# Performance work log

Hardware: AMD Instinct MI355X
Metric: run time of the kernel (lower is better)

## Reference

```python
import jax, jax.numpy as jnp
import numpy as np

N_NODES = 100000
N_EDGES = 1600000
IN_FEATS = 128
N_HIDDEN = 64
N_HEADS = 4
N_CLASSES = 16


def setup_inputs() -> dict:
    key = jax.random.key(0)
    ks = jax.random.split(key, 16)
    h = jax.random.normal(ks[0], (N_NODES, IN_FEATS), dtype=jnp.float32)
    src = jax.random.randint(ks[1], (N_EDGES,), 0, N_NODES, dtype=jnp.int32)
    dst = jax.random.randint(ks[2], (N_EDGES,), 0, N_NODES, dtype=jnp.int32)
    def xavier(k, shape, fan_in, fan_out):
        gain = jnp.sqrt(2.0)  # calculate_gain('relu')
        std = gain * jnp.sqrt(2.0 / (fan_in + fan_out))
        return (std * jax.random.normal(k, shape)).astype(jnp.float32)
    # layer 1: per-head W [H, in, out], A [H, 2*out]
    W1 = xavier(ks[3], (N_HEADS, IN_FEATS, N_HIDDEN), IN_FEATS, N_HIDDEN)
    b1 = jnp.zeros((N_HEADS, N_HIDDEN), jnp.float32)
    a1 = xavier(ks[4], (N_HEADS, 2 * N_HIDDEN), 2 * N_HIDDEN, 1)
    ab1 = jnp.zeros((N_HEADS,), jnp.float32)
    # layer 2: input is concat of heads = N_HEADS*N_HIDDEN, output n_classes, heads averaged
    d2 = N_HEADS * N_HIDDEN
    W2 = xavier(ks[5], (N_HEADS, d2, N_CLASSES), d2, N_CLASSES)
    b2 = jnp.zeros((N_HEADS, N_CLASSES), jnp.float32)
    a2 = xavier(ks[6], (N_HEADS, 2 * N_CLASSES), 2 * N_CLASSES, 1)
    ab2 = jnp.zeros((N_HEADS,), jnp.float32)
    fc_w = xavier(ks[7], (N_CLASSES, N_CLASSES), N_CLASSES, N_CLASSES)
    fc_b = jnp.zeros((N_CLASSES,), jnp.float32)
    return dict(h=h, src=src, dst=dst, W1=W1, b1=b1, a1=a1, ab1=ab1,
                W2=W2, b2=b2, a2=a2, ab2=ab2, fc_w=fc_w, fc_b=fc_b)


def gat_layer(h, src, dst, W, b, a, ab, n_nodes):
    # h: [N, F]; W: [H, F, O]; a: [H, 2O]
    O = W.shape[-1]
    Wh = jnp.einsum('nf,hfo->nho', h, W) + b          # [N, H, O]
    Wh_src = Wh[src]                                   # [E, H, O] (messages Wh_j)
    Wh_dst = Wh[dst]                                   # [E, H, O] (Wh_i)
    # e_ij = LeakyReLU(A([Wh_i, Wh_j]), 0.2)
    e = (jnp.einsum('eho,ho->eh', Wh_dst, a[:, :O])
         + jnp.einsum('eho,ho->eh', Wh_src, a[:, O:]) + ab)  # [E, H]
    e = jax.nn.leaky_relu(e, 0.2)
    # segment softmax over incoming edges of each dst node
    m = jax.ops.segment_max(e, dst, num_segments=n_nodes)     # [N, H] (-inf for empty)
    ex = jnp.exp(e - m[dst])
    denom = jax.ops.segment_sum(ex, dst, num_segments=n_nodes)
    alpha = ex / denom[dst]                                    # [E, H]
    # weighted neighbor aggregation (zero for zero-in-degree nodes, as DGL)
    out = jax.ops.segment_sum(alpha[:, :, None] * Wh_src, dst, num_segments=n_nodes)
    return out  # [N, H, O]


def reference(h, src, dst, W1, b1, a1, ab1, W2, b2, a2, ab2, fc_w, fc_b):
    n = h.shape[0]
    # layer 1 (heads concatenated) + ELU; dropout = identity (eval mode)
    h1 = gat_layer(h, src, dst, W1, b1, a1, ab1, n)            # [N, H, n_hidden]
    h1 = jax.nn.elu(h1.reshape(n, -1))                         # [N, H*n_hidden]
    # layer 2 (heads averaged) + softmax over features
    h2 = gat_layer(h1, src, dst, W2, b2, a2, ab2, n).mean(axis=1)  # [N, n_classes]
    h2 = jax.nn.softmax(h2, axis=1)
    # readout: mean over nodes, then fc
    hg = h2.mean(axis=0)                                        # [n_classes]
    return hg @ fc_w.T + fc_b
```

## Files before the change

### kernel.cpp

```cpp
#include <hip/hip_runtime.h>
#include <math.h>

#define N_NODES  100000
#define N_EDGES  1600000
#define IN_F     128
#define HID      64
#define HEADS    4
#define NCLS     16
#define D1       (HEADS*HID)
#define D2       (HEADS*NCLS)

#define RB1 128
#define AGG_BLOCKS 2048
#define AGG_WAVES  (AGG_BLOCKS * 4)
#define GEMM1_BLOCKS ((N_NODES + 63) / 64)

#define NBKT   ((N_NODES + 255) / 256)
#define BCAP   5120
#define BK_BLOCKS 256
#define BK_CHUNK  ((N_EDGES + BK_BLOCKS - 1) / BK_BLOCKS)

typedef __attribute__((ext_vector_type(8))) short bf16x8_t;
typedef __attribute__((ext_vector_type(4))) float f32x4_t;
typedef __attribute__((ext_vector_type(2))) float f32x2_t;

__device__ __forceinline__ unsigned bf16rne(float x) {
  unsigned u = __float_as_uint(x);
  return (u + 0x7fffu + ((u >> 16) & 1u)) >> 16;
}
__device__ __forceinline__ unsigned packbf2(float lo, float hi) {
  return bf16rne(lo) | (bf16rne(hi) << 16);
}
__device__ __forceinline__ f32x2_t pkfma(f32x2_t a, f32x2_t b, f32x2_t c) {
  return __builtin_elementwise_fma(a, b, c);
}

__global__ __launch_bounds__(256)
void k_prep(const float* __restrict__ W1, const float* __restrict__ W2,
            unsigned* __restrict__ W1t32, unsigned* __restrict__ W2t32,
            int* __restrict__ cursor) {
  int t = threadIdx.x;
  if (blockIdx.x == 0) {
    int c = t;
    const float* wp = W1 + ((c >> 6) << 13) + (c & 63);
    unsigned* op = W1t32 + c * 64;
    for (int fp = 0; fp < 64; ++fp) {
      float lo = wp[(2 * fp) << 6];
      float hi = wp[(2 * fp + 1) << 6];
      op[fp] = packbf2(lo, hi);
    }
  } else if (blockIdx.x == 1) {
    int c = t & 63, fq = t >> 6;
    const float* wp = W2 + ((c >> 4) << 12) + (c & 15);
    unsigned* op = W2t32 + c * 128 + fq * 32;
    for (int fp = 0; fp < 32; ++fp) {
      int f0 = fq * 64 + 2 * fp;
      op[fp] = packbf2(wp[f0 << 4], wp[(f0 + 1) << 4]);
    }
  } else {
    for (int i = t; i <= NBKT; i += 256) cursor[i] = 0;
  }
}

__global__ __launch_bounds__(256)
void k_bucket(const int* __restrict__ src, const int* __restrict__ dst,
              int* __restrict__ cursor, unsigned* __restrict__ bucketed) {
  __shared__ int dstL[BK_CHUNK];
  __shared__ int srcL[BK_CHUNK];
  __shared__ int hist[NBKT];
  __shared__ int base[NBKT];
  __shared__ int cur[NBKT];
  int t = threadIdx.x;
  int e0 = blockIdx.x * BK_CHUNK;
  int e1 = e0 + BK_CHUNK; if (e1 > N_EDGES) e1 = N_EDGES;
  int n = e1 - e0;
  for (int i = t; i < NBKT; i += 256) { hist[i] = 0; cur[i] = 0; }
  __syncthreads();
  for (int i = t; i < n; i += 256) {
    int d = dst[e0 + i];
    int s = src[e0 + i];
    dstL[i] = d;
    srcL[i] = s;
    atomicAdd(&hist[d >> 8], 1);
  }
  __syncthreads();
  for (int i = t; i < NBKT; i += 256) {
    int hv = hist[i];
    base[i] = hv ? atomicAdd(&cursor[i], hv) : 0;
  }
  __syncthreads();
  for (int i = t; i < n; i += 256) {
    int d = dstL[i];
    int b = d >> 8;
    int r = atomicAdd(&cur[b], 1);
    unsigned q = (unsigned)(base[b] + r);
    if (q < BCAP)
      bucketed[(size_t)b * BCAP + q] = ((unsigned)(d & 255) << 20) | (unsigned)srcL[i];
  }
}

__global__ __launch_bounds__(512)
void k_bscan(const int* __restrict__ cursor, int* __restrict__ bbase,
             int* __restrict__ offs) {
  __shared__ int part[512];
  int t = threadIdx.x;
  part[t] = (t < NBKT) ? cursor[t] : 0;
  __syncthreads();
  for (int o = 1; o < 512; o <<= 1) {
    int v = (t >= o) ? part[t - o] : 0;
    __syncthreads();
    part[t] += v;
    __syncthreads();
  }
  if (t < NBKT) bbase[t] = (t == 0) ? 0 : part[t - 1];
  if (t == 0) offs[N_NODES] = N_EDGES;
}

__global__ __launch_bounds__(256)
void k_b2csr(const unsigned* __restrict__ bucketed, const int* __restrict__ cursor,
             const int* __restrict__ bbase,
             int* __restrict__ offs, int* __restrict__ csrsrc) {
  __shared__ unsigned ed[BCAP];
  __shared__ int cnt[256];
  __shared__ int pfx[256];
  __shared__ int exc[256];
  __shared__ int cur[256];
  int b = blockIdx.x;
  int t = threadIdx.x;
  int n = cursor[b]; if (n > BCAP) n = BCAP;
  int gb = bbase[b];
  const unsigned* bp = bucketed + (size_t)b * BCAP;
  cnt[t] = 0;
  __syncthreads();
  for (int i = t; i < n; i += 256) {
    unsigned v = bp[i];
    ed[i] = v;
    atomicAdd(&cnt[v >> 20], 1);
  }
  __syncthreads();
  int x = cnt[t];
  pfx[t] = x;
  __syncthreads();
  for (int o = 1; o < 256; o <<= 1) {
    int v = (t >= o) ? pfx[t - o] : 0;
    __syncthreads();
    pfx[t] += v;
    __syncthreads();
  }
  int excl = pfx[t] - x;
  int node = b * 256 + t;
  if (node < N_NODES) offs[node] = gb + excl;
  exc[t] = excl;
  cur[t] = 0;
  __syncthreads();
  for (int i = t; i < n; i += 256) {
    unsigned v = ed[i];
    int d = v >> 20;
    int r = atomicAdd(&cur[d], 1);
    csrsrc[gb + exc[d] + r] = (int)(v & 0xFFFFFu);
  }
}

__global__ __launch_bounds__(256)
void k_gemm1(const float* __restrict__ h, const unsigned short* __restrict__ W1t,
             const float* __restrict__ bias, const float* __restrict__ a1,
             unsigned char* __restrict__ Wh8,
             float* __restrict__ sD, float* __restrict__ sS) {
  __shared__ float aLds[512];
  int t = threadIdx.x;
  aLds[t] = a1[t];
  aLds[t + 256] = a1[t + 256];
  __syncthreads();

  int wv = t >> 6;
  int lane = t & 63;
  int m = lane & 15;
  int q8 = (lane >> 4) * 8;
  int node = blockIdx.x * 64 + wv * 16 + m;
  int nclamp = node < N_NODES ? node : N_NODES - 1;

  f32x4_t acc[16] = {};
  const float* hp0 = h + (size_t)nclamp * IN_F + q8;
  #pragma unroll
  for (int ks = 0; ks < 4; ++ks) {
    int kk = ks * 32;
    float4 f0 = *(const float4*)(hp0 + kk);
    float4 f1 = *(const float4*)(hp0 + kk + 4);
    bf16x8_t bf;
    bf[0] = (short)bf16rne(f0.x); bf[1] = (short)bf16rne(f0.y);
    bf[2] = (short)bf16rne(f0.z); bf[3] = (short)bf16rne(f0.w);
    bf[4] = (short)bf16rne(f1.x); bf[5] = (short)bf16rne(f1.y);
    bf[6] = (short)bf16rne(f1.z); bf[7] = (short)bf16rne(f1.w);
    #pragma unroll
    for (int ct = 0; ct < 16; ++ct) {
      bf16x8_t af = *(const bf16x8_t*)(W1t + (ct * 16 + m) * IN_F + kk + q8);
      acc[ct] = __builtin_amdgcn_mfma_f32_16x16x32_bf16(af, bf, acc[ct], 0, 0, 0);
    }
  }
  if (node < N_NODES) {
    unsigned char* op = Wh8 + (size_t)node * D1;
    int quad4 = (lane >> 4) * 4;
    float pd[4] = {}, ps[4] = {};
    #pragma unroll
    for (int ct = 0; ct < 16; ++ct) {
      int c0 = ct * 16 + quad4;
      float4 bb = *(const float4*)(bias + c0);
      float v0 = acc[ct][0] + bb.x, v1 = acc[ct][1] + bb.y;
      float v2 = acc[ct][2] + bb.z, v3 = acc[ct][3] + bb.w;
      int hh = ct >> 2;
      const float* aD = &aLds[hh * 128 + (c0 & 63)];
      pd[hh] += v0 * aD[0] + v1 * aD[1] + v2 * aD[2] + v3 * aD[3];
      ps[hh] += v0 * aD[64] + v1 * aD[65] + v2 * aD[66] + v3 * aD[67];
      int pk = __builtin_amdgcn_cvt_pk_fp8_f32(v0, v1, 0, false);
      pk = __builtin_amdgcn_cvt_pk_fp8_f32(v2, v3, pk, true);
      *(unsigned*)(op + c0) = (unsigned)pk;
    }
    #pragma unroll
    for (int hh = 0; hh < 4; ++hh) {
      pd[hh] += __shfl_xor(pd[hh], 16); pd[hh] += __shfl_xor(pd[hh], 32);
      ps[hh] += __shfl_xor(ps[hh], 16); ps[hh] += __shfl_xor(ps[hh], 32);
    }
    if (lane < 16) {
      ((float4*)sD)[node] = make_float4(pd[0], pd[1], pd[2], pd[3]);
      ((float4*)sS)[node] = make_float4(ps[0], ps[1], ps[2], ps[3]);
    }
  }
}

__global__ __launch_bounds__(256)
void k_gemm2(const unsigned short* __restrict__ h1b, const unsigned short* __restrict__ W2t,
             const float* __restrict__ bias, const float* __restrict__ a2,
             unsigned short* __restrict__ Whb2,
             float* __restrict__ sD, float* __restrict__ sS) {
  __shared__ float aLds[128];
  int t = threadIdx.x;
  if (t < 128) aLds[t] = a2[t];
  __syncthreads();

  int wv = t >> 6;
  int lane = t & 63;
  int m = lane & 15;
  int q8 = (lane >> 4) * 8;
  int node = blockIdx.x * 64 + wv * 16 + m;
  int nclamp = node < N_NODES ? node : N_NODES - 1;

  f32x4_t acc[4] = {};
  const unsigned short* hp0 = h1b + (size_t)nclamp * D1 + q8;
  #pragma unroll
  for (int ks = 0; ks < 8; ++ks) {
    int kk = ks * 32;
    bf16x8_t bf = *(const bf16x8_t*)(hp0 + kk);
    #pragma unroll
    for (int ct = 0; ct < 4; ++ct) {
      bf16x8_t af = *(const bf16x8_t*)(W2t + (ct * 16 + m) * D1 + kk + q8);
      acc[ct] = __builtin_amdgcn_mfma_f32_16x16x32_bf16(af, bf, acc[ct], 0, 0, 0);
    }
  }
  if (node < N_NODES) {
    unsigned short* op = Whb2 + (size_t)node * D2;
    int quad4 = (lane >> 4) * 4;
    float pd[4] = {}, ps[4] = {};
    #pragma unroll
    for (int ct = 0; ct < 4; ++ct) {
      int c0 = ct * 16 + quad4;
      float4 bb = *(const float4*)(bias + c0);
      float v0 = acc[ct][0] + bb.x, v1 = acc[ct][1] + bb.y;
      float v2 = acc[ct][2] + bb.z, v3 = acc[ct][3] + bb.w;
      const float* aD = &aLds[ct * 32 + (c0 & 15)];
      pd[ct] += v0 * aD[0] + v1 * aD[1] + v2 * aD[2] + v3 * aD[3];
      ps[ct] += v0 * aD[16] + v1 * aD[17] + v2 * aD[18] + v3 * aD[19];
      uint2 o;
      o.x = packbf2(v0, v1);
      o.y = packbf2(v2, v3);
      *(uint2*)(op + c0) = o;
    }
    #pragma unroll
    for (int hh = 0; hh < 4; ++hh) {
      pd[hh] += __shfl_xor(pd[hh], 16); pd[hh] += __shfl_xor(pd[hh], 32);
      ps[hh] += __shfl_xor(ps[hh], 16); ps[hh] += __shfl_xor(ps[hh], 32);
    }
    if (lane < 16) {
      ((float4*)sD)[node] = make_float4(pd[0], pd[1], pd[2], pd[3]);
      ((float4*)sS)[node] = make_float4(ps[0], ps[1], ps[2], ps[3]);
    }
  }
}

__device__ __forceinline__ float lrelu(float x) { return x > 0.f ? x : 0.2f * x; }
__device__ __forceinline__ float elu(float x)   { return x > 0.f ? x : expm1f(x); }

__global__ __launch_bounds__(256)
void k_agg1(const int* __restrict__ offs, const int* __restrict__ csrsrc,
            const float* __restrict__ sD, const float* __restrict__ sS,
            const float* __restrict__ ab,
            const unsigned char* __restrict__ Wh8, unsigned short* __restrict__ h1out) {
  __shared__ float exbuf[4][64 * 4];
  __shared__ int   offbuf[4][64];
  int wv = threadIdx.x >> 6;
  int lane = threadIdx.x & 63;
  int g = lane >> 5;
  int l = lane & 31;
  int hh = l >> 3;
  unsigned lb = (unsigned)(l << 3);
  float ab0 = ab[0], ab1 = ab[1], ab2 = ab[2], ab3 = ab[3];
  const float* eb = exbuf[wv];
  const int* ob = offbuf[wv];

  for (int wid = blockIdx.x * 4 + wv; wid < N_NODES; wid += AGG_WAVES) {
    f32x2_t acc[4] = {};
    float z0 = 0.f, z1 = 0.f, z2 = 0.f, z3 = 0.f;
    int beg = offs[wid], end = offs[wid + 1];
    bool nonempty = end > beg;
    if (nonempty) {
      float4 dv = ((const float4*)sD)[wid];
      float db0 = dv.x + ab0, db1 = dv.y + ab1;
      float db2 = dv.z + ab2, db3 = dv.w + ab3;
      for (int cbeg = beg; cbeg < end; cbeg += 64) {
        int j = cbeg + lane;
        int cnt = end - cbeg; if (cnt > 64) cnt = 64;
        int sid = 0;
        float e0 = 0.f, e1 = 0.f, e2 = 0.f, e3 = 0.f;
        if (j < end) {
          sid = csrsrc[j];
          float4 sv = ((const float4*)sS)[sid];
          e0 = __expf(lrelu(db0 + sv.x));
          e1 = __expf(lrelu(db1 + sv.y));
          e2 = __expf(lrelu(db2 + sv.z));
          e3 = __expf(lrelu(db3 + sv.w));
          z0 += e0; z1 += e1; z2 += e2; z3 += e3;
        }
        offbuf[wv][lane] = sid << 8;
        *(float4*)&exbuf[wv][lane * 4] = make_float4(e0, e1, e2, e3);
        int npairs = (cnt + 1) >> 1;
        int nh = (npairs + 1) >> 1;
        for (int u = 0; u < nh; ++u) {
          int iA = 2 * u + g;
          int iB = iA + 2 * nh;
          float wA = eb[iA * 4 + hh];
          float wB = eb[iB * 4 + hh];
          unsigned vA = (unsigned)ob[iA] + lb;
          unsigned vB = (unsigned)ob[iB] + lb;
          uint2 pA = *(const uint2*)(Wh8 + vA);
          uint2 pB = *(const uint2*)(Wh8 + vB);
          f32x2_t wa2 = {wA, wA};
          acc[0] = pkfma(wa2, __builtin_amdgcn_cvt_pk_f32_fp8(pA.x, false), acc[0]);
          acc[1] = pkfma(wa2, __builtin_amdgcn_cvt_pk_f32_fp8(pA.x, true ), acc[1]);
          acc[2] = pkfma(wa2, __builtin_amdgcn_cvt_pk_f32_fp8(pA.y, false), acc[2]);
          acc[3] = pkfma(wa2, __builtin_amdgcn_cvt_pk_f32_fp8(pA.y, true ), acc[3]);
          f32x2_t wb2 = {wB, wB};
          acc[0] = pkfma(wb2, __builtin_amdgcn_cvt_pk_f32_fp8(pB.x, false), acc[0]);
          acc[1] = pkfma(wb2, __builtin_amdgcn_cvt_pk_f32_fp8(pB.x, true ), acc[1]);
          acc[2] = pkfma(wb2, __builtin_amdgcn_cvt_pk_f32_fp8(pB.y, false), acc[2]);
          acc[3] = pkfma(wb2, __builtin_amdgcn_cvt_pk_f32_fp8(pB.y, true ), acc[3]);
        }
      }
      #pragma unroll
      for (int o = 32; o; o >>= 1) {
        z0 += __shfl_xor(z0, o);
        z1 += __shfl_xor(z1, o);
        z2 += __shfl_xor(z2, o);
        z3 += __shfl_xor(z3, o);
      }
    }
    #pragma unroll
    for (int i = 0; i < 4; ++i) {
      acc[i][0] += __shfl_xor(acc[i][0], 32);
      acc[i][1] += __shfl_xor(acc[i][1], 32);
    }
    float z = (hh == 0) ? z0 : (hh == 1) ? z1 : (hh == 2) ? z2 : z3;
    if (!nonempty) z = 1.f;
    float inv = 1.f / z;
    if (g == 0) {
      uint4 o;
      o.x = packbf2(elu(acc[0][0] * inv), elu(acc[0][1] * inv));
      o.y = packbf2(elu(acc[1][0] * inv), elu(acc[1][1] * inv));
      o.z = packbf2(elu(acc[2][0] * inv), elu(acc[2][1] * inv));
      o.w = packbf2(elu(acc[3][0] * inv), elu(acc[3][1] * inv));
      *(uint4*)(h1out + (size_t)wid * D1 + l * 8) = o;
    }
  }
}

__global__ __launch_bounds__(256)
void k_agg2(const int* __restrict__ offs, const int* __restrict__ csrsrc,
            const float* __restrict__ sD, const float* __restrict__ sS,
            const float* __restrict__ ab,
            const unsigned short* __restrict__ Whb2, float* __restrict__ partials) {
  __shared__ float exbuf[4][64 * 4];
  __shared__ int   offbuf[4][64];
  __shared__ float red[4][16];
  int wv = threadIdx.x >> 6;
  int lane = threadIdx.x & 63;
  int g = lane >> 4;
  int l = lane & 15;
  int hh = l >> 2;
  unsigned lb = (unsigned)(l << 3);
  float ab0 = ab[0], ab1 = ab[1], ab2 = ab[2], ab3 = ab[3];
  const float* eb = exbuf[wv];
  const int* ob = offbuf[wv];
  float smacc[4] = {};

  for (int wid = blockIdx.x * 4 + wv; wid < N_NODES; wid += AGG_WAVES) {
    f32x2_t acc[2] = {};
    float z0 = 0.f, z1 = 0.f, z2 = 0.f, z3 = 0.f;
    int beg = offs[wid], end = offs[wid + 1];
    bool nonempty = end > beg;
    if (nonempty) {
      float4 dv = ((const float4*)sD)[wid];
      float db0 = dv.x + ab0, db1 = dv.y + ab1;
      float db2 = dv.z + ab2, db3 = dv.w + ab3;
      for (int cbeg = beg; cbeg < end; cbeg += 64) {
        int j = cbeg + lane;
        int cnt = end - cbeg; if (cnt > 64) cnt = 64;
        int sid = 0;
        float e0 = 0.f, e1 = 0.f, e2 = 0.f, e3 = 0.f;
        if (j < end) {
          sid = csrsrc[j];
          float4 sv = ((const float4*)sS)[sid];
          e0 = __expf(lrelu(db0 + sv.x));
          e1 = __expf(lrelu(db1 + sv.y));
          e2 = __expf(lrelu(db2 + sv.z));
          e3 = __expf(lrelu(db3 + sv.w));
          z0 += e0; z1 += e1; z2 += e2; z3 += e3;
        }
        offbuf[wv][lane] = sid << 7;
        *(float4*)&exbuf[wv][lane * 4] = make_float4(e0, e1, e2, e3);
        int ni = (cnt + 3) >> 2;
        int nh2 = (ni + 1) >> 1;
        for (int it = 0; it < nh2; ++it) {
          int qA = 4 * it + g;
          int qB = qA + 4 * nh2;
          float wA = eb[qA * 4 + hh];
          float wB = eb[qB * 4 + hh];
          unsigned vA = (unsigned)ob[qA] + lb;
          unsigned vB = (unsigned)ob[qB] + lb;
          uint2 pA = *(const uint2*)((const unsigned char*)Whb2 + vA);
          uint2 pB = *(const uint2*)((const unsigned char*)Whb2 + vB);
          f32x2_t wa2 = {wA, wA};
          f32x2_t dA0, dA1;
          dA0[0] = __uint_as_float(pA.x << 16); dA0[1] = __uint_as_float(pA.x & 0xffff0000u);
          dA1[0] = __uint_as_float(pA.y << 16); dA1[1] = __uint_as_float(pA.y & 0xffff0000u);
          acc[0] = pkfma(wa2, dA0, acc[0]);
          acc[1] = pkfma(wa2, dA1, acc[1]);
          f32x2_t wb2 = {wB, wB};
          f32x2_t dB0, dB1;
          dB0[0] = __uint_as_float(pB.x << 16); dB0[1] = __uint_as_float(pB.x & 0xffff0000u);
          dB1[0] = __uint_as_float(pB.y << 16); dB1[1] = __uint_as_float(pB.y & 0xffff0000u);
          acc[0] = pkfma(wb2, dB0, acc[0]);
          acc[1] = pkfma(wb2, dB1, acc[1]);
        }
      }
      #pragma unroll
      for (int s = 32; s; s >>= 1) {
        z0 += __shfl_xor(z0, s);
        z1 += __shfl_xor(z1, s);
        z2 += __shfl_xor(z2, s);
        z3 += __shfl_xor(z3, s);
      }
    }
    #pragma unroll
    for (int i = 0; i < 2; ++i) {
      acc[i][0] += __shfl_xor(acc[i][0], 16);
      acc[i][1] += __shfl_xor(acc[i][1], 16);
      acc[i][0] += __shfl_xor(acc[i][0], 32);
      acc[i][1] += __shfl_xor(acc[i][1], 32);
    }
    float z = (hh == 0) ? z0 : (hh == 1) ? z1 : (hh == 2) ? z2 : z3;
    if (!nonempty) z = 1.f;
    float inv = 1.f / z;
    float val[4];
    val[0] = acc[0][0] * inv;
    val[1] = acc[0][1] * inv;
    val[2] = acc[1][0] * inv;
    val[3] = acc[1][1] * inv;
    #pragma unroll
    for (int i = 0; i < 4; ++i) {
      val[i] += __shfl_xor(val[i], 4);
      val[i] += __shfl_xor(val[i], 8);
      val[i] *= 0.25f;
    }
    float mx = fmaxf(fmaxf(val[0], val[1]), fmaxf(val[2], val[3]));
    mx = fmaxf(mx, __shfl_xor(mx, 1));
    mx = fmaxf(mx, __shfl_xor(mx, 2));
    float e[4];
    float ssum = 0.f;
    #pragma unroll
    for (int i = 0; i < 4; ++i) { e[i] = __expf(val[i] - mx); ssum += e[i]; }
    ssum += __shfl_xor(ssum, 1);
    ssum += __shfl_xor(ssum, 2);
    float rinv = 1.f / ssum;
    #pragma unroll
    for (int i = 0; i < 4; ++i) smacc[i] += e[i] * rinv;
  }

  if (g == 0 && l < 4) {
    #pragma unroll
    for (int i = 0; i < 4; ++i) red[wv][l * 4 + i] = smacc[i];
  }
  __syncthreads();
  if (threadIdx.x < 16) {
    partials[(size_t)blockIdx.x * 16 + threadIdx.x] =
        red[0][threadIdx.x] + red[1][threadIdx.x] +
        red[2][threadIdx.x] + red[3][threadIdx.x];
  }
}

__global__ __launch_bounds__(256)
void k_reduce1(const float* __restrict__ partials, int nrows,
               float* __restrict__ out) {
  __shared__ float red[16][17];
  int t = threadIdx.x;
  int c = t & 15, rl = t >> 4;
  int per = (nrows + RB1 - 1) / RB1;
  int rbeg = blockIdx.x * per;
  int rend = rbeg + per; if (rend > nrows) rend = nrows;
  float s = 0.f;
  for (int r = rbeg + rl; r < rend; r += 16) s += partials[(size_t)r * 16 + c];
  red[rl][c] = s;
  __syncthreads();
  for (int st = 8; st; st >>= 1) {
    if (rl < st) red[rl][c] += red[rl + st][c];
    __syncthreads();
  }
  if (t < 16) out[(size_t)blockIdx.x * 16 + t] = red[0][t];
}

__global__ __launch_bounds__(256)
void k_final(const float* __restrict__ partials,
             const float* __restrict__ fcw, const float* __restrict__ fcb,
             float* __restrict__ out) {
  __shared__ float red[16][17];
  __shared__ float hg[16];
  int t = threadIdx.x;
  int c = t & 15, rl = t >> 4;
  float s = 0.f;
  for (int r = rl; r < RB1; r += 16) s += partials[(size_t)r * 16 + c];
  red[rl][c] = s;
  __syncthreads();
  for (int st = 8; st; st >>= 1) {
    if (rl < st) red[rl][c] += red[rl + st][c];
    __syncthreads();
  }
  if (t < 16) hg[t] = red[0][t] * (1.0f / N_NODES);
  __syncthreads();
  if (t < 16) {
    float acc = fcb[t];
    #pragma unroll
    for (int k = 0; k < 16; ++k) acc += hg[k] * fcw[t * 16 + k];
    out[t] = acc;
  }
}

extern "C" void kernel_launch(void* const* d_in, const int* in_sizes, int n_in,
                              void* d_out, int out_size, void* d_ws, size_t ws_size,
                              hipStream_t stream) {
  const float* h   = (const float*)d_in[0];
  const int*   src = (const int*)  d_in[1];
  const int*   dst = (const int*)  d_in[2];
  const float* W1  = (const float*)d_in[3];
  const float* b1  = (const float*)d_in[4];
  const float* a1  = (const float*)d_in[5];
  const float* ab1 = (const float*)d_in[6];
  const float* W2  = (const float*)d_in[7];
  const float* b2  = (const float*)d_in[8];
  const float* a2  = (const float*)d_in[9];
  const float* ab2 = (const float*)d_in[10];
  const float* fcw = (const float*)d_in[11];
  const float* fcb = (const float*)d_in[12];
  float* out = (float*)d_out;

  char* ws = (char*)d_ws;
  size_t off = 0;
  auto alloc = [&](size_t bytes) -> char* {
    char* p = ws + off;
    off += (bytes + 255) & ~(size_t)255;
    return p;
  };
  unsigned char*  Wh8  = (unsigned char*)alloc((size_t)N_NODES * D1);
  unsigned short* h1b  = (unsigned short*)alloc((size_t)N_NODES * D1 * 2);
  unsigned short* Whb2 = (unsigned short*)alloc((size_t)N_NODES * D2 * 2);
  unsigned short* W1t  = (unsigned short*)alloc((size_t)D1 * IN_F * 2);
  unsigned short* W2t  = (unsigned short*)alloc((size_t)D2 * D1 * 2);
  float* sD1 = (float*)alloc((size_t)N_NODES * 4 * 4);
  float* sS1 = (float*)alloc((size_t)N_NODES * 4 * 4);
  float* sD2 = (float*)alloc((size_t)N_NODES * 4 * 4);
  float* sS2 = (float*)alloc((size_t)N_NODES * 4 * 4);
  int* cursor   = (int*)alloc((size_t)(NBKT + 1) * 4);
  unsigned* bucketed = (unsigned*)alloc((size_t)NBKT * BCAP * 4);
  int* bbase  = (int*)alloc((size_t)NBKT * 4);
  int* offs   = (int*)alloc((size_t)(N_NODES + 1) * 4);
  int* csrsrc = (int*)alloc((size_t)N_EDGES * 4);
  float* partials  = (float*)alloc((size_t)AGG_BLOCKS * 16 * 4);
  float* partials2 = (float*)alloc((size_t)RB1 * 16 * 4);

  k_prep<<<3, 256, 0, stream>>>(W1, W2, (unsigned*)W1t, (unsigned*)W2t, cursor);

  k_bucket<<<BK_BLOCKS, 256, 0, stream>>>(src, dst, cursor, bucketed);

  k_gemm1<<<GEMM1_BLOCKS, 256, 0, stream>>>(h, W1t, b1, a1, Wh8, sD1, sS1);

  k_bscan<<<1, 512, 0, stream>>>(cursor, bbase, offs);
  k_b2csr<<<NBKT, 256, 0, stream>>>(bucketed, cursor, bbase, offs, csrsrc);

  k_agg1<<<AGG_BLOCKS, 256, 0, stream>>>(offs, csrsrc, sD1, sS1, ab1, Wh8, h1b);

  k_gemm2<<<GEMM1_BLOCKS, 256, 0, stream>>>(h1b, W2t, b2, a2, Whb2, sD2, sS2);
  k_agg2<<<AGG_BLOCKS, 256, 0, stream>>>(offs, csrsrc, sD2, sS2, ab2, Whb2, partials);

  k_reduce1<<<RB1, 256, 0, stream>>>(partials, AGG_BLOCKS, partials2);
  k_final<<<1, 256, 0, stream>>>(partials2, fcw, fcb, out);
}
```

Measured before the change: 409.4 us.

## Eliminate scan and reduce kernels by folding work into neighbouring launches

Removes the single-block bucket-scan kernel: each b2csr block now computes its own bucket base by summing the preceding cursor counts with a block reduction, and the offs sentinel is written in k_prep. The two-stage final reduction is merged into one single-block kernel that reads all aggregation partials directly. k_bucket moves to 1024-thread blocks and rereads src/dst from global memory in place of staging them in shared memory. Together these cut two kernel launches and their serialization gaps, at the cost of redundant prefix sums per block, a longer serial final reduction, and a second global read of the edge arrays.

```diff
diff --git a/kernel.cpp b/kernel.cpp
--- a/kernel.cpp
+++ b/kernel.cpp
@@ -10,7 +10,6 @@
 #define D1       (HEADS*HID)
 #define D2       (HEADS*NCLS)
 
-#define RB1 128
 #define AGG_BLOCKS 2048
 #define AGG_WAVES  (AGG_BLOCKS * 4)
 #define GEMM1_BLOCKS ((N_NODES + 63) / 64)
@@ -38,7 +37,7 @@
 __global__ __launch_bounds__(256)
 void k_prep(const float* __restrict__ W1, const float* __restrict__ W2,
             unsigned* __restrict__ W1t32, unsigned* __restrict__ W2t32,
-            int* __restrict__ cursor) {
+            int* __restrict__ cursor, int* __restrict__ offs) {
   int t = threadIdx.x;
   if (blockIdx.x == 0) {
     int c = t;
@@ -59,14 +58,13 @@
     }
   } else {
     for (int i = t; i <= NBKT; i += 256) cursor[i] = 0;
-  }
-}
-
-__global__ __launch_bounds__(256)
+    if (t == 0) offs[N_NODES] = N_EDGES;
+  }
+}
+
+__global__ __launch_bounds__(1024)
 void k_bucket(const int* __restrict__ src, const int* __restrict__ dst,
               int* __restrict__ cursor, unsigned* __restrict__ bucketed) {
-  __shared__ int dstL[BK_CHUNK];
-  __shared__ int srcL[BK_CHUNK];
   __shared__ int hist[NBKT];
   __shared__ int base[NBKT];
   __shared__ int cur[NBKT];
@@ -74,64 +72,50 @@
   int e0 = blockIdx.x * BK_CHUNK;
   int e1 = e0 + BK_CHUNK; if (e1 > N_EDGES) e1 = N_EDGES;
   int n = e1 - e0;
-  for (int i = t; i < NBKT; i += 256) { hist[i] = 0; cur[i] = 0; }
-  __syncthreads();
-  for (int i = t; i < n; i += 256) {
+  for (int i = t; i < NBKT; i += 1024) { hist[i] = 0; cur[i] = 0; }
+  __syncthreads();
+  for (int i = t; i < n; i += 1024)
+    atomicAdd(&hist[dst[e0 + i] >> 8], 1);
+  __syncthreads();
+  for (int i = t; i < NBKT; i += 1024) {
+    int hv = hist[i];
+    base[i] = hv ? atomicAdd(&cursor[i], hv) : 0;
+  }
+  __syncthreads();
+  for (int i = t; i < n; i += 1024) {
     int d = dst[e0 + i];
     int s = src[e0 + i];
-    dstL[i] = d;
-    srcL[i] = s;
-    atomicAdd(&hist[d >> 8], 1);
-  }
-  __syncthreads();
-  for (int i = t; i < NBKT; i += 256) {
-    int hv = hist[i];
-    base[i] = hv ? atomicAdd(&cursor[i], hv) : 0;
-  }
-  __syncthreads();
-  for (int i = t; i < n; i += 256) {
-    int d = dstL[i];
     int b = d >> 8;
     int r = atomicAdd(&cur[b], 1);
     unsigned q = (unsigned)(base[b] + r);
     if (q < BCAP)
-      bucketed[(size_t)b * BCAP + q] = ((unsigned)(d & 255) << 20) | (unsigned)srcL[i];
-  }
-}
-
-__global__ __launch_bounds__(512)
-void k_bscan(const int* __restrict__ cursor, int* __restrict__ bbase,
-             int* __restrict__ offs) {
-  __shared__ int part[512];
-  int t = threadIdx.x;
-  part[t] = (t < NBKT) ? cursor[t] : 0;
-  __syncthreads();
-  for (int o = 1; o < 512; o <<= 1) {
-    int v = (t >= o) ? part[t - o] : 0;
-    __syncthreads();
-    part[t] += v;
-    __syncthreads();
-  }
-  if (t < NBKT) bbase[t] = (t == 0) ? 0 : part[t - 1];
-  if (t == 0) offs[N_NODES] = N_EDGES;
+      bucketed[(size_t)b * BCAP + q] = ((unsigned)(d & 255) << 20) | (unsigned)s;
+  }
 }
 
 __global__ __launch_bounds__(256)
 void k_b2csr(const unsigned* __restrict__ bucketed, const int* __restrict__ cursor,
-             const int* __restrict__ bbase,
              int* __restrict__ offs, int* __restrict__ csrsrc) {
   __shared__ unsigned ed[BCAP];
+  __shared__ int redsum[256];
   __shared__ int cnt[256];
   __shared__ int pfx[256];
   __shared__ int exc[256];
   __shared__ int cur[256];
   int b = blockIdx.x;
   int t = threadIdx.x;
+  int s = 0;
+  for (int i = t; i < b; i += 256) s += cursor[i];
+  redsum[t] = s;
+  cnt[t] = 0;
+  __syncthreads();
+  for (int st = 128; st; st >>= 1) {
+    if (t < st) redsum[t] += redsum[t + st];
+    __syncthreads();
+  }
+  int gb = redsum[0];
   int n = cursor[b]; if (n > BCAP) n = BCAP;
-  int gb = bbase[b];
   const unsigned* bp = bucketed + (size_t)b * BCAP;
-  cnt[t] = 0;
-  __syncthreads();
   for (int i = t; i < n; i += 256) {
     unsigned v = bp[i];
     ed[i] = v;
@@ -506,35 +490,15 @@
 }
 
 __global__ __launch_bounds__(256)
-void k_reduce1(const float* __restrict__ partials, int nrows,
-               float* __restrict__ out) {
-  __shared__ float red[16][17];
-  int t = threadIdx.x;
-  int c = t & 15, rl = t >> 4;
-  int per = (nrows + RB1 - 1) / RB1;
-  int rbeg = blockIdx.x * per;
-  int rend = rbeg + per; if (rend > nrows) rend = nrows;
-  float s = 0.f;
-  for (int r = rbeg + rl; r < rend; r += 16) s += partials[(size_t)r * 16 + c];
-  red[rl][c] = s;
-  __syncthreads();
-  for (int st = 8; st; st >>= 1) {
-    if (rl < st) red[rl][c] += red[rl + st][c];
-    __syncthreads();
-  }
-  if (t < 16) out[(size_t)blockIdx.x * 16 + t] = red[0][t];
-}
-
-__global__ __launch_bounds__(256)
-void k_final(const float* __restrict__ partials,
-             const float* __restrict__ fcw, const float* __restrict__ fcb,
-             float* __restrict__ out) {
+void k_reduce(const float* __restrict__ partials,
+              const float* __restrict__ fcw, const float* __restrict__ fcb,
+              float* __restrict__ out) {
   __shared__ float red[16][17];
   __shared__ float hg[16];
   int t = threadIdx.x;
   int c = t & 15, rl = t >> 4;
   float s = 0.f;
-  for (int r = rl; r < RB1; r += 16) s += partials[(size_t)r * 16 + c];
+  for (int r = rl; r < AGG_BLOCKS; r += 16) s += partials[(size_t)r * 16 + c];
   red[rl][c] = s;
   __syncthreads();
   for (int st = 8; st; st >>= 1) {
@@ -587,26 +551,22 @@
   float* sS2 = (float*)alloc((size_t)N_NODES * 4 * 4);
   int* cursor   = (int*)alloc((size_t)(NBKT + 1) * 4);
   unsigned* bucketed = (unsigned*)alloc((size_t)NBKT * BCAP * 4);
-  int* bbase  = (int*)alloc((size_t)NBKT * 4);
   int* offs   = (int*)alloc((size_t)(N_NODES + 1) * 4);
   int* csrsrc = (int*)alloc((size_t)N_EDGES * 4);
   float* partials  = (float*)alloc((size_t)AGG_BLOCKS * 16 * 4);
-  float* partials2 = (float*)alloc((size_t)RB1 * 16 * 4);
-
-  k_prep<<<3, 256, 0, stream>>>(W1, W2, (unsigned*)W1t, (unsigned*)W2t, cursor);
-
-  k_bucket<<<BK_BLOCKS, 256, 0, stream>>>(src, dst, cursor, bucketed);
+
+  k_prep<<<3, 256, 0, stream>>>(W1, W2, (unsigned*)W1t, (unsigned*)W2t, cursor, offs);
+
+  k_bucket<<<BK_BLOCKS, 1024, 0, stream>>>(src, dst, cursor, bucketed);
 
   k_gemm1<<<GEMM1_BLOCKS, 256, 0, stream>>>(h, W1t, b1, a1, Wh8, sD1, sS1);
 
-  k_bscan<<<1, 512, 0, stream>>>(cursor, bbase, offs);
-  k_b2csr<<<NBKT, 256, 0, stream>>>(bucketed, cursor, bbase, offs, csrsrc);
+  k_b2csr<<<NBKT, 256, 0, stream>>>(bucketed, cursor, offs, csrsrc);
 
   k_agg1<<<AGG_BLOCKS, 256, 0, stream>>>(offs, csrsrc, sD1, sS1, ab1, Wh8, h1b);
 
   k_gemm2<<<GEMM1_BLOCKS, 256, 0, stream>>>(h1b, W2t, b2, a2, Whb2, sD2, sS2);
   k_agg2<<<AGG_BLOCKS, 256, 0, stream>>>(offs, csrsrc, sD2, sS2, ab2, Whb2, partials);
 
-  k_reduce1<<<RB1, 256, 0, stream>>>(partials, AGG_BLOCKS, partials2);
-  k_final<<<1, 256, 0, stream>>>(partials2, fcw, fcb, out);
-}
+  k_reduce<<<1, 256, 0, stream>>>(partials, fcw, fcb, out);
+}
```

After: 430.5 us. 1.05x slower.
